# Kernel optimization log

Measured on AMD Instinct MI355X. Metric: run time of the kernel, lower is better.

Reference implementation:

```python
import jax, jax.numpy as jnp
import numpy as np

NUM_EXPERTS = 8
IN_FEATURES = 2048
OUT_FEATURES = 2048
TOTAL_TOKENS = 16384


def setup_inputs() -> dict:
    key = jax.random.key(0)
    kx, kc, kw, kb = jax.random.split(key, 4)
    X = jax.random.normal(kx, (TOTAL_TOKENS, IN_FEATURES), dtype=jnp.float32)
    # expert_offset: [E+1] monotonically increasing segment boundaries,
    # offset[0] = 0, offset[E] = TOTAL_TOKENS (tokens pre-sorted by expert).
    cuts = jnp.sort(jax.random.randint(kc, (NUM_EXPERTS - 1,), 0, TOTAL_TOKENS))
    expert_offset = jnp.concatenate([
        jnp.zeros((1,), dtype=jnp.int64),
        cuts.astype(jnp.int64),
        jnp.full((1,), TOTAL_TOKENS, dtype=jnp.int64),
    ])
    weight = jax.random.normal(kw, (NUM_EXPERTS, OUT_FEATURES, IN_FEATURES), dtype=jnp.float32) * 0.02
    bias = jax.random.normal(kb, (NUM_EXPERTS, OUT_FEATURES), dtype=jnp.float32) * 0.02
    return {"X": X, "expert_offset": expert_offset, "weight": weight, "bias": bias}


def reference(X, expert_offset, weight, bias):
    # X: [T, in], weight: [E, out, in], bias: [E, out]
    T = X.shape[0]
    E = weight.shape[0]
    # token t belongs to expert e iff offset[e] <= t < offset[e+1]
    eid = jnp.searchsorted(expert_offset[1:], jnp.arange(T), side="right")  # [T]
    Y = bias[eid]  # [T, out] per-token expert bias
    # grouped GEMM expressed as E masked dense GEMMs (E is a small fixed constant)
    for e in range(E):
        mask = (eid == e).astype(X.dtype)[:, None]  # [T, 1]
        Y = Y + mask * (X @ weight[e].T)
    return Y
```

## Files before the change

### kernel.cpp

```cpp
#include <hip/hip_runtime.h>


typedef __attribute__((ext_vector_type(8))) short s16x8;
typedef __attribute__((ext_vector_type(4))) short s16x4;
typedef __attribute__((ext_vector_type(4))) float f32x4;

typedef __attribute__((address_space(1))) void gv_t;
typedef __attribute__((address_space(3))) void lv_t;

#define PBM 256
#define PBN 128
#define PBK 32
#define PTHREADS 512
#define ASLOT (PBM * PBK)
#define BSLOT (PBN * PBK)

#define FBM 128
#define FBN 128
#define FBK 32
#define LDK 40

__device__ __forceinline__ short f2bf(float f) {
    union { float f; unsigned u; } v; v.f = f;
    unsigned r = v.u + 0x7FFFu + ((v.u >> 16) & 1u);
    return (short)(r >> 16);
}

__device__ __forceinline__ long long load_off(const void* p, int i, bool i64) {
    if (i64) return ((const long long*)p)[i];
    return (long long)((const int*)p)[i];
}

__global__ __launch_bounds__(256)
void cvt_kernel(const float* __restrict__ src, short* __restrict__ dst, int n4) {
    int i = blockIdx.x * 256 + threadIdx.x;
    if (i >= n4) return;
    float4 v = ((const float4*)src)[i];
    s16x4 b;
    b.x = f2bf(v.x); b.y = f2bf(v.y); b.z = f2bf(v.z); b.w = f2bf(v.w);
    ((s16x4*)dst)[i] = b;
}

__device__ __forceinline__ bool sched_tile(const void* offp, bool off_i64, int NEXP,
                                           int slot, int bm,
                                           int& e_out, long long& row0, int& rows) {
    int acc_t = 0;
    for (int e = 0; e < NEXP; ++e) {
        long long s = load_off(offp, e, off_i64);
        long long t = load_off(offp, e + 1, off_i64);
        int n = (int)(t - s);
        int nt = (n + bm - 1) / bm;
        if (slot < acc_t + nt) {
            int lt = slot - acc_t;
            row0 = s + (long long)lt * bm;
            rows = (int)(t - row0);
            if (rows > bm) rows = bm;
            e_out = e;
            return true;
        }
        acc_t += nt;
    }
    return false;
}

__global__ __launch_bounds__(PTHREADS, 2)
void moe_gemm_bf16_pipe(const short* __restrict__ Xb16,
                        const void* __restrict__ offp,
                        const short* __restrict__ Wb16,
                        const float* __restrict__ Bias,
                        float* __restrict__ Y,
                        int IN_F, int OUT_F, int NEXP, int Ttot) {
    const bool off_i64 = (((const int*)offp)[NEXP] != Ttot);

    int e_found; long long row0; int rows;
    if (!sched_tile(offp, off_i64, NEXP, blockIdx.y, PBM, e_found, row0, rows)) return;

    const int n0 = blockIdx.x * PBN;
    const int tid = threadIdx.x;
    const int wave = tid >> 6;
    const int lane = tid & 63;
    const int wm = (wave >> 1) * 64;
    const int wn = (wave & 1) * 64;
    const int lrow = lane & 15;
    const int kg = lane >> 4;
    const int sw = (lrow >> 1) & 3;

    __shared__ __align__(16) short As[4 * ASLOT];
    __shared__ __align__(16) short Bs[4 * BSLOT];

    const short* Xb = Xb16 + (size_t)row0 * IN_F;
    const short* Wb = Wb16 + (size_t)e_found * OUT_F * IN_F + (size_t)n0 * IN_F;

    const int lr4 = lane >> 2;
    const int colOff = ((lane & 3) ^ ((lr4 >> 1) & 3)) * 8;
    const int ra0 = wave * 16 + lr4;
    const int ra1 = 128 + wave * 16 + lr4;
    const int ra0c = ra0 < rows ? ra0 : rows - 1;
    const int ra1c = ra1 < rows ? ra1 : rows - 1;
    const int rb = wave * 16 + lr4;

    const short* srcA0 = Xb + (size_t)ra0c * IN_F + colOff;
    const short* srcA1 = Xb + (size_t)ra1c * IN_F + colOff;
    const short* srcB  = Wb + (size_t)rb * IN_F + colOff;
    const int dA0 = wave * 512;
    const int dA1 = (8 + wave) * 512;
    const int dB  = wave * 512;

    const int nkt = IN_F / PBK;

    auto STAGE = [&](int kt_) {
        const int s_ = kt_ & 3;
        const int ko_ = kt_ * PBK;
        __builtin_amdgcn_global_load_lds((gv_t*)(srcA0 + ko_),
                                         (lv_t*)(As + s_ * ASLOT + dA0), 16, 0, 0);
        __builtin_amdgcn_global_load_lds((gv_t*)(srcA1 + ko_),
                                         (lv_t*)(As + s_ * ASLOT + dA1), 16, 0, 0);
        __builtin_amdgcn_global_load_lds((gv_t*)(srcB + ko_),
                                         (lv_t*)(Bs + s_ * BSLOT + dB), 16, 0, 0);
    };

    STAGE(0);
    if (nkt > 1) STAGE(1);
    if (nkt > 2) STAGE(2);

    f32x4 acc[4][4] = {};

    for (int kt = 0; kt < nkt; ++kt) {
        if (kt + 2 < nkt)      asm volatile("s_waitcnt vmcnt(6)" ::: "memory");
        else if (kt + 1 < nkt) asm volatile("s_waitcnt vmcnt(3)" ::: "memory");
        else                   asm volatile("s_waitcnt vmcnt(0)" ::: "memory");
        asm volatile("s_barrier" ::: "memory");

        if (kt + 3 < nkt) STAGE(kt + 3);

        const short* aS = As + (kt & 3) * ASLOT;
        const short* bS = Bs + (kt & 3) * BSLOT;
        s16x8 af[4], bf[4];
        #pragma unroll
        for (int i = 0; i < 4; ++i)
            af[i] = *(const s16x8*)&aS[(wm + i * 16 + lrow) * PBK + ((kg ^ sw) * 8)];
        #pragma unroll
        for (int j = 0; j < 4; ++j)
            bf[j] = *(const s16x8*)&bS[(wn + j * 16 + lrow) * PBK + ((kg ^ sw) * 8)];

        __builtin_amdgcn_s_setprio(1);
        #pragma unroll
        for (int i = 0; i < 4; ++i)
            #pragma unroll
            for (int j = 0; j < 4; ++j)
                acc[i][j] = __builtin_amdgcn_mfma_f32_16x16x32_bf16(
                    af[i], bf[j], acc[i][j], 0, 0, 0);
        __builtin_amdgcn_s_setprio(0);
    }

    float bv[4];
    #pragma unroll
    for (int j = 0; j < 4; ++j)
        bv[j] = Bias[(size_t)e_found * OUT_F + n0 + wn + j * 16 + lrow];

    #pragma unroll
    for (int i = 0; i < 4; ++i) {
        #pragma unroll
        for (int r = 0; r < 4; ++r) {
            int rr = wm + i * 16 + kg * 4 + r;
            if (rr < rows) {
                float* yrow = Y + (size_t)(row0 + rr) * OUT_F + n0;
                #pragma unroll
                for (int j = 0; j < 4; ++j)
                    yrow[wn + j * 16 + lrow] = acc[i][j][r] + bv[j];
            }
        }
    }
}

__global__ __launch_bounds__(256, 2)
void moe_gemm_f32(const float* __restrict__ X,
                  const void* __restrict__ offp,
                  const float* __restrict__ W,
                  const float* __restrict__ Bias,
                  float* __restrict__ Y,
                  int IN_F, int OUT_F, int NEXP, int Ttot) {
    const bool off_i64 = (((const int*)offp)[NEXP] != Ttot);
    int e_found; long long row0; int rows;
    if (!sched_tile(offp, off_i64, NEXP, blockIdx.y, FBM, e_found, row0, rows)) return;

    const int n0 = blockIdx.x * FBN;
    const int tid = threadIdx.x;
    const int wave = tid >> 6;
    const int lane = tid & 63;
    const int wm = (wave & 1) * 64;
    const int wn = (wave >> 1) * 64;
    const int lrow = lane & 15;
    const int kg = lane >> 4;

    __shared__ __align__(16) short As[FBM][LDK];
    __shared__ __align__(16) short Bs[FBN][LDK];

    const float* Xb = X + (size_t)row0 * IN_F;
    const float* Wb = W + (size_t)e_found * OUT_F * IN_F + (size_t)n0 * IN_F;

    f32x4 acc[4][4] = {};

    for (int k0 = 0; k0 < IN_F; k0 += FBK) {
        __syncthreads();
        #pragma unroll
        for (int p = 0; p < 4; ++p) {
            int idx = p * 256 + tid;
            int r = idx >> 3;
            int kc = (idx & 7) << 2;
            float4 v = make_float4(0.f, 0.f, 0.f, 0.f);
            if (r < rows) v = *(const float4*)(Xb + (size_t)r * IN_F + k0 + kc);
            s16x4 b;
            b.x = f2bf(v.x); b.y = f2bf(v.y); b.z = f2bf(v.z); b.w = f2bf(v.w);
            *(s16x4*)&As[r][kc] = b;
        }
        #pragma unroll
        for (int p = 0; p < 4; ++p) {
            int idx = p * 256 + tid;
            int r = idx >> 3;
            int kc = (idx & 7) << 2;
            float4 v = *(const float4*)(Wb + (size_t)r * IN_F + k0 + kc);
            s16x4 b;
            b.x = f2bf(v.x); b.y = f2bf(v.y); b.z = f2bf(v.z); b.w = f2bf(v.w);
            *(s16x4*)&Bs[r][kc] = b;
        }
        __syncthreads();

        s16x8 af[4], bf[4];
        #pragma unroll
        for (int i = 0; i < 4; ++i)
            af[i] = *(const s16x8*)&As[wm + i * 16 + lrow][kg * 8];
        #pragma unroll
        for (int j = 0; j < 4; ++j)
            bf[j] = *(const s16x8*)&Bs[wn + j * 16 + lrow][kg * 8];

        #pragma unroll
        for (int i = 0; i < 4; ++i)
            #pragma unroll
            for (int j = 0; j < 4; ++j)
                acc[i][j] = __builtin_amdgcn_mfma_f32_16x16x32_bf16(
                    af[i], bf[j], acc[i][j], 0, 0, 0);
    }

    float bv[4];
    #pragma unroll
    for (int j = 0; j < 4; ++j)
        bv[j] = Bias[(size_t)e_found * OUT_F + n0 + wn + j * 16 + lrow];

    #pragma unroll
    for (int i = 0; i < 4; ++i) {
        #pragma unroll
        for (int r = 0; r < 4; ++r) {
            int rr = wm + i * 16 + kg * 4 + r;
            if (rr < rows) {
                float* yrow = Y + (size_t)(row0 + rr) * OUT_F + n0;
                #pragma unroll
                for (int j = 0; j < 4; ++j)
                    yrow[wn + j * 16 + lrow] = acc[i][j][r] + bv[j];
            }
        }
    }
}

extern "C" void kernel_launch(void* const* d_in, const int* in_sizes, int n_in,
                              void* d_out, int out_size, void* d_ws, size_t ws_size,
                              hipStream_t stream) {
    const float* X = (const float*)d_in[0];
    const void* off = d_in[1];
    const float* W = (const float*)d_in[2];
    const float* Bias = (const float*)d_in[3];
    float* Y = (float*)d_out;

    const int NEXP1 = in_sizes[1];
    const int NEXP = NEXP1 - 1;
    const int OUT_F = in_sizes[3] / NEXP;
    const int IN_F = (int)((long long)in_sizes[2] / NEXP / OUT_F);
    const int T = in_sizes[0] / IN_F;

    const long long Xn = (long long)T * IN_F;
    const long long Wn = (long long)NEXP * OUT_F * IN_F;
    const size_t need = (size_t)(Xn + Wn) * sizeof(short);

    const bool shape_ok = (OUT_F % PBN == 0) && (IN_F % PBK == 0) &&
                          (Xn % 4 == 0) && (Wn % 4 == 0);

    if (shape_ok && ws_size >= need) {
        short* wsX = (short*)d_ws;
        short* wsW = wsX + Xn;
        {
            int n4 = (int)(Xn / 4);
            cvt_kernel<<<(n4 + 255) / 256, 256, 0, stream>>>(X, wsX, n4);
        }
        {
            int n4 = (int)(Wn / 4);
            cvt_kernel<<<(n4 + 255) / 256, 256, 0, stream>>>(W, wsW, n4);
        }
        const int maxRowTiles = T / PBM + NEXP;
        dim3 grid(OUT_F / PBN, maxRowTiles);
        moe_gemm_bf16_pipe<<<grid, PTHREADS, 0, stream>>>(wsX, off, wsW, Bias, Y,
                                                          IN_F, OUT_F, NEXP, T);
    } else {
        const int maxRowTiles = T / FBM + NEXP;
        dim3 grid(OUT_F / FBN, maxRowTiles);
        moe_gemm_f32<<<grid, 256, 0, stream>>>(X, off, W, Bias, Y,
                                               IN_F, OUT_F, NEXP, T);
    }
}
```

Measured before the change: 613.2 us.

## Enlarge GEMM tile to 256x256 with interleaved prefetch and grid-stride convert

Doubles the N tile of the grouped bf16 GEMM to 256, giving each wave a 128x64 output block of 8x4 MFMA accumulators so every loaded B fragment is reused across more A rows. The next-stage global-to-LDS loads are spread between the LDS fragment reads and MFMA groups instead of being issued all at once. The fp32-to-bf16 convert kernels become grid-stride loops with a capped block count. The larger tile doubles LDS use and accumulator registers, which can lower occupancy, and halves the number of column blocks, so fewer workgroups are launched.

```diff
diff --git a/kernel.cpp b/kernel.cpp
--- a/kernel.cpp
+++ b/kernel.cpp
@@ -8,12 +8,12 @@
 typedef __attribute__((address_space(1))) void gv_t;
 typedef __attribute__((address_space(3))) void lv_t;
 
-#define PBM 256
-#define PBN 128
-#define PBK 32
-#define PTHREADS 512
-#define ASLOT (PBM * PBK)
-#define BSLOT (PBN * PBK)
+#define QBM 256
+#define QBN 256
+#define QBK 32
+#define QTHREADS 512
+#define QASLOT (QBM * QBK)
+#define QBSLOT (QBN * QBK)
 
 #define FBM 128
 #define FBN 128
@@ -32,13 +32,14 @@
 }
 
 __global__ __launch_bounds__(256)
-void cvt_kernel(const float* __restrict__ src, short* __restrict__ dst, int n4) {
-    int i = blockIdx.x * 256 + threadIdx.x;
-    if (i >= n4) return;
-    float4 v = ((const float4*)src)[i];
-    s16x4 b;
-    b.x = f2bf(v.x); b.y = f2bf(v.y); b.z = f2bf(v.z); b.w = f2bf(v.w);
-    ((s16x4*)dst)[i] = b;
+void cvt_kernel(const float* __restrict__ src, short* __restrict__ dst, long long n4) {
+    long long stride = (long long)gridDim.x * 256;
+    for (long long i = (long long)blockIdx.x * 256 + threadIdx.x; i < n4; i += stride) {
+        float4 v = ((const float4*)src)[i];
+        s16x4 b;
+        b.x = f2bf(v.x); b.y = f2bf(v.y); b.z = f2bf(v.z); b.w = f2bf(v.w);
+        ((s16x4*)dst)[i] = b;
+    }
 }
 
 __device__ __forceinline__ bool sched_tile(const void* offp, bool off_i64, int NEXP,
@@ -63,30 +64,30 @@
     return false;
 }
 
-__global__ __launch_bounds__(PTHREADS, 2)
-void moe_gemm_bf16_pipe(const short* __restrict__ Xb16,
-                        const void* __restrict__ offp,
-                        const short* __restrict__ Wb16,
-                        const float* __restrict__ Bias,
-                        float* __restrict__ Y,
-                        int IN_F, int OUT_F, int NEXP, int Ttot) {
+__global__ __launch_bounds__(QTHREADS, 2)
+void moe_gemm_bf16_256(const short* __restrict__ Xb16,
+                       const void* __restrict__ offp,
+                       const short* __restrict__ Wb16,
+                       const float* __restrict__ Bias,
+                       float* __restrict__ Y,
+                       int IN_F, int OUT_F, int NEXP, int Ttot) {
     const bool off_i64 = (((const int*)offp)[NEXP] != Ttot);
 
     int e_found; long long row0; int rows;
-    if (!sched_tile(offp, off_i64, NEXP, blockIdx.y, PBM, e_found, row0, rows)) return;
-
-    const int n0 = blockIdx.x * PBN;
+    if (!sched_tile(offp, off_i64, NEXP, blockIdx.y, QBM, e_found, row0, rows)) return;
+
+    const int n0 = blockIdx.x * QBN;
     const int tid = threadIdx.x;
     const int wave = tid >> 6;
     const int lane = tid & 63;
-    const int wm = (wave >> 1) * 64;
-    const int wn = (wave & 1) * 64;
+    const int wm = (wave >> 2) * 128;
+    const int wn = (wave & 3) * 64;
     const int lrow = lane & 15;
     const int kg = lane >> 4;
-    const int sw = (lrow >> 1) & 3;
-
-    __shared__ __align__(16) short As[4 * ASLOT];
-    __shared__ __align__(16) short Bs[4 * BSLOT];
+    const int swr = (lrow >> 1) & 3;
+
+    __shared__ __align__(16) short As[4 * QASLOT];
+    __shared__ __align__(16) short Bs[4 * QBSLOT];
 
     const short* Xb = Xb16 + (size_t)row0 * IN_F;
     const short* Wb = Wb16 + (size_t)e_found * OUT_F * IN_F + (size_t)n0 * IN_F;
@@ -101,55 +102,96 @@
 
     const short* srcA0 = Xb + (size_t)ra0c * IN_F + colOff;
     const short* srcA1 = Xb + (size_t)ra1c * IN_F + colOff;
-    const short* srcB  = Wb + (size_t)rb * IN_F + colOff;
+    const short* srcB0 = Wb + (size_t)rb * IN_F + colOff;
+    const short* srcB1 = Wb + (size_t)(128 + rb) * IN_F + colOff;
     const int dA0 = wave * 512;
-    const int dA1 = (8 + wave) * 512;
-    const int dB  = wave * 512;
-
-    const int nkt = IN_F / PBK;
-
-    auto STAGE = [&](int kt_) {
-        const int s_ = kt_ & 3;
-        const int ko_ = kt_ * PBK;
-        __builtin_amdgcn_global_load_lds((gv_t*)(srcA0 + ko_),
-                                         (lv_t*)(As + s_ * ASLOT + dA0), 16, 0, 0);
-        __builtin_amdgcn_global_load_lds((gv_t*)(srcA1 + ko_),
-                                         (lv_t*)(As + s_ * ASLOT + dA1), 16, 0, 0);
-        __builtin_amdgcn_global_load_lds((gv_t*)(srcB + ko_),
-                                         (lv_t*)(Bs + s_ * BSLOT + dB), 16, 0, 0);
+    const int dA1 = 4096 + wave * 512;
+    const int dB0 = wave * 512;
+    const int dB1 = 4096 + wave * 512;
+
+    const int nkt = IN_F / QBK;
+
+    auto ST_A0 = [&](int kt_) {
+        __builtin_amdgcn_global_load_lds((gv_t*)(srcA0 + (size_t)kt_ * QBK),
+                                         (lv_t*)(As + (kt_ & 3) * QASLOT + dA0), 16, 0, 0);
     };
-
-    STAGE(0);
-    if (nkt > 1) STAGE(1);
-    if (nkt > 2) STAGE(2);
-
-    f32x4 acc[4][4] = {};
+    auto ST_A1 = [&](int kt_) {
+        __builtin_amdgcn_global_load_lds((gv_t*)(srcA1 + (size_t)kt_ * QBK),
+                                         (lv_t*)(As + (kt_ & 3) * QASLOT + dA1), 16, 0, 0);
+    };
+    auto ST_B0 = [&](int kt_) {
+        __builtin_amdgcn_global_load_lds((gv_t*)(srcB0 + (size_t)kt_ * QBK),
+                                         (lv_t*)(Bs + (kt_ & 3) * QBSLOT + dB0), 16, 0, 0);
+    };
+    auto ST_B1 = [&](int kt_) {
+        __builtin_amdgcn_global_load_lds((gv_t*)(srcB1 + (size_t)kt_ * QBK),
+                                         (lv_t*)(Bs + (kt_ & 3) * QBSLOT + dB1), 16, 0, 0);
+    };
+
+    ST_A0(0); ST_A1(0); ST_B0(0); ST_B1(0);
+    if (nkt > 1) { ST_A0(1); ST_A1(1); ST_B0(1); ST_B1(1); }
+    if (nkt > 2) { ST_A0(2); ST_A1(2); ST_B0(2); ST_B1(2); }
+
+    f32x4 acc[8][4] = {};
 
     for (int kt = 0; kt < nkt; ++kt) {
-        if (kt + 2 < nkt)      asm volatile("s_waitcnt vmcnt(6)" ::: "memory");
-        else if (kt + 1 < nkt) asm volatile("s_waitcnt vmcnt(3)" ::: "memory");
+        if (kt + 2 < nkt)      asm volatile("s_waitcnt vmcnt(8)" ::: "memory");
+        else if (kt + 1 < nkt) asm volatile("s_waitcnt vmcnt(4)" ::: "memory");
         else                   asm volatile("s_waitcnt vmcnt(0)" ::: "memory");
         asm volatile("s_barrier" ::: "memory");
 
-        if (kt + 3 < nkt) STAGE(kt + 3);
-
-        const short* aS = As + (kt & 3) * ASLOT;
-        const short* bS = Bs + (kt & 3) * BSLOT;
-        s16x8 af[4], bf[4];
-        #pragma unroll
-        for (int i = 0; i < 4; ++i)
-            af[i] = *(const s16x8*)&aS[(wm + i * 16 + lrow) * PBK + ((kg ^ sw) * 8)];
+        const bool pf = (kt + 3 < nkt);
+        const int kp = kt + 3;
+        const short* aS = As + (kt & 3) * QASLOT;
+        const short* bS = Bs + (kt & 3) * QBSLOT;
+
+        s16x8 bfr[4];
         #pragma unroll
         for (int j = 0; j < 4; ++j)
-            bf[j] = *(const s16x8*)&bS[(wn + j * 16 + lrow) * PBK + ((kg ^ sw) * 8)];
-
+            bfr[j] = *(const s16x8*)&bS[(wn + j * 16 + lrow) * QBK + ((kg ^ swr) * 8)];
+        if (pf) ST_A0(kp);
+
+        s16x8 af0 = *(const s16x8*)&aS[(wm + 0 * 16 + lrow) * QBK + ((kg ^ swr) * 8)];
+        s16x8 af1 = *(const s16x8*)&aS[(wm + 1 * 16 + lrow) * QBK + ((kg ^ swr) * 8)];
+        if (pf) ST_A1(kp);
         __builtin_amdgcn_s_setprio(1);
         #pragma unroll
-        for (int i = 0; i < 4; ++i)
-            #pragma unroll
-            for (int j = 0; j < 4; ++j)
-                acc[i][j] = __builtin_amdgcn_mfma_f32_16x16x32_bf16(
-                    af[i], bf[j], acc[i][j], 0, 0, 0);
+        for (int j = 0; j < 4; ++j) {
+            acc[0][j] = __builtin_amdgcn_mfma_f32_16x16x32_bf16(af0, bfr[j], acc[0][j], 0, 0, 0);
+            acc[1][j] = __builtin_amdgcn_mfma_f32_16x16x32_bf16(af1, bfr[j], acc[1][j], 0, 0, 0);
+        }
+        __builtin_amdgcn_s_setprio(0);
+
+        s16x8 af2 = *(const s16x8*)&aS[(wm + 2 * 16 + lrow) * QBK + ((kg ^ swr) * 8)];
+        s16x8 af3 = *(const s16x8*)&aS[(wm + 3 * 16 + lrow) * QBK + ((kg ^ swr) * 8)];
+        if (pf) ST_B0(kp);
+        __builtin_amdgcn_s_setprio(1);
+        #pragma unroll
+        for (int j = 0; j < 4; ++j) {
+            acc[2][j] = __builtin_amdgcn_mfma_f32_16x16x32_bf16(af2, bfr[j], acc[2][j], 0, 0, 0);
+            acc[3][j] = __builtin_amdgcn_mfma_f32_16x16x32_bf16(af3, bfr[j], acc[3][j], 0, 0, 0);
+        }
+        __builtin_amdgcn_s_setprio(0);
+
+        s16x8 af4 = *(const s16x8*)&aS[(wm + 4 * 16 + lrow) * QBK + ((kg ^ swr) * 8)];
+        s16x8 af5 = *(const s16x8*)&aS[(wm + 5 * 16 + lrow) * QBK + ((kg ^ swr) * 8)];
+        if (pf) ST_B1(kp);
+        __builtin_amdgcn_s_setprio(1);
+        #pragma unroll
+        for (int j = 0; j < 4; ++j) {
+            acc[4][j] = __builtin_amdgcn_mfma_f32_16x16x32_bf16(af4, bfr[j], acc[4][j], 0, 0, 0);
+            acc[5][j] = __builtin_amdgcn_mfma_f32_16x16x32_bf16(af5, bfr[j], acc[5][j], 0, 0, 0);
+        }
+        __builtin_amdgcn_s_setprio(0);
+
+        s16x8 af6 = *(const s16x8*)&aS[(wm + 6 * 16 + lrow) * QBK + ((kg ^ swr) * 8)];
+        s16x8 af7 = *(const s16x8*)&aS[(wm + 7 * 16 + lrow) * QBK + ((kg ^ swr) * 8)];
+        __builtin_amdgcn_s_setprio(1);
+        #pragma unroll
+        for (int j = 0; j < 4; ++j) {
+            acc[6][j] = __builtin_amdgcn_mfma_f32_16x16x32_bf16(af6, bfr[j], acc[6][j], 0, 0, 0);
+            acc[7][j] = __builtin_amdgcn_mfma_f32_16x16x32_bf16(af7, bfr[j], acc[7][j], 0, 0, 0);
+        }
         __builtin_amdgcn_s_setprio(0);
     }
 
@@ -159,7 +201,7 @@
         bv[j] = Bias[(size_t)e_found * OUT_F + n0 + wn + j * 16 + lrow];
 
     #pragma unroll
-    for (int i = 0; i < 4; ++i) {
+    for (int i = 0; i < 8; ++i) {
         #pragma unroll
         for (int r = 0; r < 4; ++r) {
             int rr = wm + i * 16 + kg * 4 + r;
@@ -281,24 +323,26 @@
     const long long Wn = (long long)NEXP * OUT_F * IN_F;
     const size_t need = (size_t)(Xn + Wn) * sizeof(short);
 
-    const bool shape_ok = (OUT_F % PBN == 0) && (IN_F % PBK == 0) &&
+    const bool shape_ok = (OUT_F % QBN == 0) && (IN_F % QBK == 0) && (IN_F >= 3 * QBK) &&
                           (Xn % 4 == 0) && (Wn % 4 == 0);
 
     if (shape_ok && ws_size >= need) {
         short* wsX = (short*)d_ws;
         short* wsW = wsX + Xn;
         {
-            int n4 = (int)(Xn / 4);
-            cvt_kernel<<<(n4 + 255) / 256, 256, 0, stream>>>(X, wsX, n4);
+            long long n4 = Xn / 4;
+            int blks = (int)((n4 + 255) / 256); if (blks > 4096) blks = 4096;
+            cvt_kernel<<<blks, 256, 0, stream>>>(X, wsX, n4);
         }
         {
-            int n4 = (int)(Wn / 4);
-            cvt_kernel<<<(n4 + 255) / 256, 256, 0, stream>>>(W, wsW, n4);
-        }
-        const int maxRowTiles = T / PBM + NEXP;
-        dim3 grid(OUT_F / PBN, maxRowTiles);
-        moe_gemm_bf16_pipe<<<grid, PTHREADS, 0, stream>>>(wsX, off, wsW, Bias, Y,
-                                                          IN_F, OUT_F, NEXP, T);
+            long long n4 = Wn / 4;
+            int blks = (int)((n4 + 255) / 256); if (blks > 4096) blks = 4096;
+            cvt_kernel<<<blks, 256, 0, stream>>>(W, wsW, n4);
+        }
+        const int maxRowTiles = T / QBM + NEXP;
+        dim3 grid(OUT_F / QBN, maxRowTiles);
+        moe_gemm_bf16_256<<<grid, QTHREADS, 0, stream>>>(wsX, off, wsW, Bias, Y,
+                                                         IN_F, OUT_F, NEXP, T);
     } else {
         const int maxRowTiles = T / FBM + NEXP;
         dim3 grid(OUT_F / FBN, maxRowTiles);
```

Measured after the change: 572.7 us. 1.07x faster.
